# Performance work log

Hardware: AMD Instinct MI355X
Metric: run time of the kernel (lower is better)

Reference implementation:

```python
import jax, jax.numpy as jnp
import numpy as np

IFZ = 256      # in_features
SFZ = 1280     # sequence_features
AHZ = 8        # attention heads
AFZ = 64       # attention feature dim per head
NRES = 20      # canonical_num_residues
SCALE = float(np.sqrt(AFZ))
RESID = float(np.sqrt(2.0))
EPS = 1e-6


def _ln(x, s, b, eps=1e-5):
    m = jnp.mean(x, axis=-1, keepdims=True)
    v = jnp.var(x, axis=-1, keepdims=True)
    return (x - m) / jnp.sqrt(v + eps) * s + b


def setup_inputs() -> dict:
    key = jax.random.key(0)
    ks = jax.random.split(key, 20)
    N, B, S = 4096, 4, 512
    HD = AHZ * AFZ
    w = lambda k, shp: (jax.random.normal(k, shp, jnp.float32) * 0.02)
    d = {}
    d["x"] = jax.random.normal(ks[0], (N, IFZ), jnp.float32)
    d["packed_sequence_emb"] = jax.random.normal(ks[1], (B, S, SFZ), jnp.float32)
    d["packed_sequence_mask"] = jnp.ones((B, S), jnp.float32)
    d["prot_mask"] = jnp.arange(N, dtype=jnp.int32)
    d["batch"] = jax.random.randint(ks[2], (N,), 0, B, jnp.int32)
    # projections (bias=False)
    d["Wq"] = w(ks[3], (HD, IFZ))
    d["Wk"] = w(ks[4], (HD, SFZ))
    d["Wv"] = w(ks[5], (HD, SFZ))
    # ag: LayerNorm(HD) -> Linear(HD, IFZ, bias=False) (dropout = identity at eval)
    d["ag_ln_s"] = jnp.ones((HD,), jnp.float32)
    d["ag_ln_b"] = jnp.zeros((HD,), jnp.float32)
    d["Wag"] = w(ks[6], (IFZ, HD))
    d["res_ln_s"] = jnp.ones((3, IFZ), jnp.float32)
    d["res_ln_b"] = jnp.zeros((3, IFZ), jnp.float32)
    d["res_w1"] = w(ks[7], (3, IFZ, IFZ))
    d["res_b1"] = jnp.zeros((3, IFZ), jnp.float32)
    d["res_w2"] = w(ks[8], (3, IFZ, IFZ))
    d["res_b2"] = jnp.zeros((3, IFZ), jnp.float32)
    d["head_w"] = w(ks[9], (NRES, IFZ))
    d["head_b"] = jnp.zeros((NRES,), jnp.float32)
    # output LayerNorm en
    d["en_s"] = jnp.ones((IFZ,), jnp.float32)
    d["en_b"] = jnp.zeros((IFZ,), jnp.float32)
    return d


def _forward(x, emb, mask, prot_mask, batch, Wq, Wk, Wv, ag_ln_s, ag_ln_b, Wag,
             res_ln_s, res_ln_b, res_w1, res_b1, res_w2, res_b2,
             head_w, head_b, en_s, en_b):
    N = x.shape[0]
    B, S = emb.shape[:2]
    b_idx = batch[prot_mask]                      # [M]
    xp = x[prot_mask]                             # [M, IFZ]
    M = xp.shape[0]
    q = (xp @ Wq.T).reshape(M, AHZ, AFZ)          # [M,H,D]
    k = (emb @ Wk.T).reshape(B, S, AHZ, AFZ)      # [B,S,H,D]
    v = (emb @ Wv.T).reshape(B, S, AHZ, AFZ)
    # score vs every protein, then pick own protein (avoids materializing [M,S,H,D] gather)
    scores_all = jnp.einsum('mhd,bshd->mbsh', q, k) / SCALE          # [M,B,S,H]
    sel = b_idx[:, None, None, None]
    scores = jnp.take_along_axis(scores_all, sel, axis=1)[:, 0]       # [M,S,H]
    mb = mask[b_idx][:, :, None]                                      # [M,S,1]
    # padded_sequence_softmax: softmax over S, zero pads, renormalize
    sm = jax.nn.softmax(scores, axis=1) * mb
    w = sm / (jnp.sum(sm, axis=1, keepdims=True) + EPS)               # [M,S,H]
    feat_all = jnp.einsum('msh,bshd->mbhd', w, v)                     # [M,B,H,D]
    feat = jnp.take_along_axis(feat_all, sel, axis=1)[:, 0]
    feat = feat.reshape(M, AHZ * AFZ)
    ag = _ln(feat, ag_ln_s, ag_ln_b) @ Wag.T                          # [M, IFZ]
    # seq_aa_head on the scattered new features (identical to ag for unique prot_mask)
    h = ag
    for i in range(3):
        y = _ln(h, res_ln_s[i], res_ln_b[i])
        y = jax.nn.relu(y @ res_w1[i].T + res_b1[i])
        y = y @ res_w2[i].T + res_b2[i]
        h = (h + y) / RESID
    logits = h @ head_w.T + head_b                                     # [M, NRES]
    new_features = jnp.zeros_like(x).at[prot_mask].set(ag)
    seq_aa_logits = jnp.zeros((N, NRES), x.dtype).at[prot_mask].set(logits)
    unpacked_scores = jnp.zeros((N, S, AHZ), x.dtype).at[prot_mask].set(scores)
    out_x = _ln(x + new_features / RESID, en_s, en_b)
    return out_x, seq_aa_logits, unpacked_scores


def reference(x, packed_sequence_emb, packed_sequence_mask, prot_mask, batch,
              Wq, Wk, Wv, ag_ln_s, ag_ln_b, Wag,
              res_ln_s, res_ln_b, res_w1, res_b1, res_w2, res_b2,
              head_w, head_b, en_s, en_b):
    return _forward(x, packed_sequence_emb, packed_sequence_mask, prot_mask, batch,
                    Wq, Wk, Wv, ag_ln_s, ag_ln_b, Wag,
                    res_ln_s, res_ln_b, res_w1, res_b1, res_w2, res_b2,
                    head_w, head_b, en_s, en_b)
```

## Files before the change

### kernel.cpp

```cpp
#include <hip/hip_runtime.h>
#include <math.h>


typedef short bf8 __attribute__((ext_vector_type(8)));
typedef short bf4 __attribute__((ext_vector_type(4)));
typedef float f32x4 __attribute__((ext_vector_type(4)));
typedef unsigned short u16;

constexpr int LDT = 40;
enum { EPI_NONE = 0, EPI_BIAS_RELU = 1, EPI_BIAS = 2, EPI_RESID = 3 };
#define RSQRT2 0.70710678118654752f

__device__ __forceinline__ u16 f2bf(float f) {
  unsigned int u = __builtin_bit_cast(unsigned int, f);
  unsigned int r = u + 0x7fffu + ((u >> 16) & 1u);
  return (u16)(r >> 16);
}
__device__ __forceinline__ float bf2f(u16 v) {
  return __builtin_bit_cast(float, (unsigned int)v << 16);
}
__device__ __forceinline__ f32x4 mfma16(bf8 a, bf8 b, f32x4 c) {
  return __builtin_amdgcn_mfma_f32_16x16x32_bf16(a, b, c, 0, 0, 0);
}

struct CvtDesc { const float* src; u16* dst; int n; };
struct CvtArgs { CvtDesc d[8]; };

__global__ __launch_bounds__(256) void cvt_k(CvtArgs a) {
  CvtDesc d = a.d[blockIdx.z];
  int i = (blockIdx.x * 256 + threadIdx.x) * 8;
  if (i >= d.n) return;
  f32x4 v0 = *(const f32x4*)(d.src + i);
  f32x4 v1 = *(const f32x4*)(d.src + i + 4);
  bf8 o;
  o[0] = (short)f2bf(v0[0]); o[1] = (short)f2bf(v0[1]);
  o[2] = (short)f2bf(v0[2]); o[3] = (short)f2bf(v0[3]);
  o[4] = (short)f2bf(v1[0]); o[5] = (short)f2bf(v1[1]);
  o[6] = (short)f2bf(v1[2]); o[7] = (short)f2bf(v1[3]);
  *(bf8*)(d.dst + i) = o;
}

template <int EPI, bool BFOUT, int MT>
__global__ __launch_bounds__(256) void mgemm2(
    const u16* __restrict__ A, const u16* __restrict__ B,
    void* __restrict__ Cv, int M, int N, int K, int lda, int ldb, int ldc,
    const float* __restrict__ bias, const float* __restrict__ Hin,
    const int* __restrict__ gatherA, const int* __restrict__ scatterC) {
  constexpr int NF = MT / 32;
  __shared__ __align__(16) u16 As[MT * LDT];
  __shared__ __align__(16) u16 Bs[64 * LDT];
  const int tid = threadIdx.x;
  const int m0 = blockIdx.y * MT, n0 = blockIdx.x * 64;
  const int wave = tid >> 6, lane = tid & 63;
  const int wm = (wave & 1) * (MT / 2), wn = (wave >> 1) * 32;
  const int lrow = lane & 15, quad = lane >> 4;
  const int srow = tid >> 2, skq = tid & 3;

  int gr0 = m0 + srow;
  int ar0 = (gr0 < M) ? (gatherA ? gatherA[gr0] : gr0) : -1;
  const u16* Ap0 = (ar0 >= 0) ? A + (size_t)ar0 * lda + skq * 8 : nullptr;
  const u16* Ap1 = nullptr;
  if constexpr (MT == 128) {
    int gr1 = m0 + srow + 64;
    int ar1 = (gr1 < M) ? (gatherA ? gatherA[gr1] : gr1) : -1;
    Ap1 = (ar1 >= 0) ? A + (size_t)ar1 * lda + skq * 8 : nullptr;
  }
  const u16* Bp = (n0 + srow < N) ? B + (size_t)(n0 + srow) * ldb + skq * 8 : nullptr;
  u16* AsW0 = &As[srow * LDT + skq * 8];
  u16* AsW1 = (MT == 128) ? &As[(srow + 64) * LDT + skq * 8] : nullptr;
  u16* BsW = &Bs[srow * LDT + skq * 8];

  f32x4 acc[NF][2];
#pragma unroll
  for (int i = 0; i < NF; ++i)
#pragma unroll
    for (int j = 0; j < 2; ++j) acc[i][j] = (f32x4){0.f, 0.f, 0.f, 0.f};
  const bf8 z8 = {0, 0, 0, 0, 0, 0, 0, 0};

  for (int k0 = 0; k0 < K; k0 += 32) {
    bf8 a0 = Ap0 ? *(const bf8*)(Ap0 + k0) : z8;
    bf8 bv = Bp ? *(const bf8*)(Bp + k0) : z8;
    *(bf8*)AsW0 = a0;
    if constexpr (MT == 128) {
      bf8 a1 = Ap1 ? *(const bf8*)(Ap1 + k0) : z8;
      *(bf8*)AsW1 = a1;
    }
    *(bf8*)BsW = bv;
    __syncthreads();
    bf8 af[NF], bfr[2];
#pragma unroll
    for (int i = 0; i < NF; ++i)
      af[i] = *(const bf8*)&As[(wm + i * 16 + lrow) * LDT + quad * 8];
#pragma unroll
    for (int j = 0; j < 2; ++j)
      bfr[j] = *(const bf8*)&Bs[(wn + j * 16 + lrow) * LDT + quad * 8];
#pragma unroll
    for (int i = 0; i < NF; ++i)
#pragma unroll
      for (int j = 0; j < 2; ++j) acc[i][j] = mfma16(af[i], bfr[j], acc[i][j]);
    __syncthreads();
  }

  float* Cf = (float*)Cv;
  u16* Cb = (u16*)Cv;
#pragma unroll
  for (int i = 0; i < NF; ++i) {
#pragma unroll
    for (int r = 0; r < 4; ++r) {
      int row = m0 + wm + i * 16 + quad * 4 + r;
      if (row >= M) continue;
      if (gatherA && gatherA[row] < 0) continue;
      int orow = scatterC ? scatterC[row] : row;
#pragma unroll
      for (int j = 0; j < 2; ++j) {
        int col = n0 + wn + j * 16 + lrow;
        if (col >= N) continue;
        float v = acc[i][j][r];
        if (EPI == EPI_BIAS_RELU) v = fmaxf(v + bias[col], 0.f);
        else if (EPI == EPI_BIAS) v += bias[col];
        else if (EPI == EPI_RESID) v = (Hin[(size_t)row * ldc + col] + v + bias[col]) * RSQRT2;
        if (BFOUT) Cb[(size_t)orow * ldc + col] = f2bf(v);
        else Cf[(size_t)orow * ldc + col] = v;
      }
    }
  }
}

__global__ __launch_bounds__(256) void vtrans(const u16* __restrict__ KV,
                                              u16* __restrict__ VT) {
  __shared__ u16 t[32][33];
  int b = blockIdx.z;
  int s0 = blockIdx.x * 32, d0 = blockIdx.y * 32;
  int tx = threadIdx.x & 31, ty = threadIdx.x >> 5;
#pragma unroll
  for (int i = 0; i < 32; i += 8)
    t[ty + i][tx] = KV[(size_t)(b * 512 + s0 + ty + i) * 1024 + 512 + d0 + tx];
  __syncthreads();
#pragma unroll
  for (int i = 0; i < 32; i += 8)
    VT[(size_t)(b * 512 + d0 + ty + i) * 512 + s0 + tx] = t[tx][ty + i];
}

constexpr int WST = 520;
constexpr int QST = 72;

__global__ __launch_bounds__(256) void attn_fused(
    const u16* __restrict__ Q, const u16* __restrict__ KV,
    const u16* __restrict__ VT, const int* __restrict__ list,
    const float* __restrict__ mask, u16* __restrict__ packed,
    u16* __restrict__ feat, int N) {
  const int NMT = gridDim.x;
  const int lin = blockIdx.y * NMT + blockIdx.x;
  const int xcd = lin & 7, rest = lin >> 3;
  const int mt = rest % NMT;
  const int y = ((rest / NMT) << 3) | xcd;
  const int b = y >> 3, h = y & 7;
  const int* lst = list + (size_t)b * N + mt * 32;
  if (lst[0] < 0) return;

  __shared__ __align__(16) u16 Ws[32 * WST];
  __shared__ __align__(16) u16 Qs[32 * QST];
  __shared__ __align__(16) u16 KVs[64 * QST];
  __shared__ __align__(16) float mk[8][68];
  __shared__ int mS[32];

  const int tid = threadIdx.x;
  const int wave = tid >> 6, lane = tid & 63;
  const int wm = (wave & 1) * 16, wns = (wave >> 1) * 32;
  const int lrow = lane & 15, quad = lane >> 4;
  const bf8 z8 = {0, 0, 0, 0, 0, 0, 0, 0};

  const int c0 = tid * 2, c1 = tid * 2 + 1;
  const int sr0 = c0 >> 3, kq0 = c0 & 7;
  const int sr1 = c1 >> 3, kq1 = c1 & 7;
  u16* kvw0 = &KVs[sr0 * QST + kq0 * 8];
  u16* kvw1 = &KVs[sr1 * QST + kq1 * 8];

  if (tid < 32) mS[tid] = lst[tid];
  {
    int p = tid >> 5, j = (tid & 31) * 2;
    *(float2*)&mk[p][j] = *(const float2*)&mask[(size_t)b * 512 + p * 64 + j];
  }
  {
    int qr = tid >> 3, kq = tid & 7;
    int m = lst[qr];
    *(bf8*)&Qs[qr * QST + kq * 8] =
        (m >= 0) ? *(const bf8*)(Q + (size_t)m * 512 + h * 64 + kq * 8) : z8;
  }
  const u16* KVb = KV + (size_t)(b * 512) * 1024 + h * 64;
  {
    int sta = mt & 7;
    *(bf8*)kvw0 = *(const bf8*)(KVb + (size_t)(sta * 64 + sr0) * 1024 + kq0 * 8);
    *(bf8*)kvw1 = *(const bf8*)(KVb + (size_t)(sta * 64 + sr1) * 1024 + kq1 * 8);
  }
  __syncthreads();

  const bf8 qa0 = *(const bf8*)&Qs[(wm + lrow) * QST + 0 + quad * 8];
  const bf8 qa1 = *(const bf8*)&Qs[(wm + lrow) * QST + 32 + quad * 8];

  bf8 r0, r1;
  for (int st = 0; st < 8; ++st) {
    const int sta = (st + mt) & 7;
    if (st < 7) {
      int nx = (st + 1 + mt) & 7;
      r0 = *(const bf8*)(KVb + (size_t)(nx * 64 + sr0) * 1024 + kq0 * 8);
      r1 = *(const bf8*)(KVb + (size_t)(nx * 64 + sr1) * 1024 + kq1 * 8);
    }
    f32x4 acc0 = {0.f, 0.f, 0.f, 0.f}, acc1 = acc0;
    {
      bf8 b00 = *(const bf8*)&KVs[(wns + lrow) * QST + quad * 8];
      bf8 b10 = *(const bf8*)&KVs[(wns + 16 + lrow) * QST + quad * 8];
      bf8 b01 = *(const bf8*)&KVs[(wns + lrow) * QST + 32 + quad * 8];
      bf8 b11 = *(const bf8*)&KVs[(wns + 16 + lrow) * QST + 32 + quad * 8];
      __builtin_amdgcn_s_setprio(1);
      acc0 = mfma16(qa0, b00, acc0);
      acc1 = mfma16(qa0, b10, acc1);
      acc0 = mfma16(qa1, b01, acc0);
      acc1 = mfma16(qa1, b11, acc1);
      __builtin_amdgcn_s_setprio(0);
    }
#pragma unroll
    for (int r = 0; r < 4; ++r) {
      int lr = wm + quad * 4 + r;
      Ws[lr * WST + sta * 64 + wns + lrow] = f2bf(acc0[r] * 0.125f);
      Ws[lr * WST + sta * 64 + wns + 16 + lrow] = f2bf(acc1[r] * 0.125f);
    }
    __syncthreads();
    if (st < 7) {
      *(bf8*)kvw0 = r0;
      *(bf8*)kvw1 = r1;
      __syncthreads();
    }
  }

  const u16* VTb = VT + (size_t)(b * 512 + h * 64) * 512;
  bf8 v0p = *(const bf8*)(VTb + (size_t)sr0 * 512 + ((mt & 7) << 6) + kq0 * 8);
  bf8 v1p = *(const bf8*)(VTb + (size_t)sr1 * 512 + ((mt & 7) << 6) + kq1 * 8);

  {
    const int row = tid >> 3, part = tid & 7;
    u16* wrow = &Ws[row * WST + part * 64];
    const int mm = mS[row];
    bf8 w[8];
    float mx = -1e30f;
#pragma unroll
    for (int v = 0; v < 8; ++v) {
      w[v] = *(const bf8*)(wrow + v * 8);
#pragma unroll
      for (int j = 0; j < 8; ++j) mx = fmaxf(mx, bf2f((u16)w[v][j]));
    }
    if (mm >= 0) {
      u16* prow = packed + ((size_t)h * N + mm) * 512 + part * 64;
#pragma unroll
      for (int v = 0; v < 8; ++v) *(bf8*)(prow + v * 8) = w[v];
    }
#pragma unroll
    for (int d = 1; d < 8; d <<= 1) mx = fmaxf(mx, __shfl_xor(mx, d));
    float ev[64];
    float se = 0.f, ms = 0.f;
#pragma unroll
    for (int v = 0; v < 8; ++v) {
      f32x4 m0 = *(const f32x4*)&mk[part][v * 8];
      f32x4 m1 = *(const f32x4*)&mk[part][v * 8 + 4];
#pragma unroll
      for (int j = 0; j < 8; ++j) {
        float e = __expf(bf2f((u16)w[v][j]) - mx);
        ev[v * 8 + j] = e;
        se += e;
        ms += e * (j < 4 ? m0[j] : m1[j - 4]);
      }
    }
#pragma unroll
    for (int d = 1; d < 8; d <<= 1) {
      se += __shfl_xor(se, d);
      ms += __shfl_xor(ms, d);
    }
    float iv = 1.0f / (ms + 1e-6f * se);
#pragma unroll
    for (int v = 0; v < 8; ++v) {
      f32x4 m0 = *(const f32x4*)&mk[part][v * 8];
      f32x4 m1 = *(const f32x4*)&mk[part][v * 8 + 4];
      bf8 o;
#pragma unroll
      for (int j = 0; j < 8; ++j)
        o[j] = (short)f2bf(ev[v * 8 + j] * (j < 4 ? m0[j] : m1[j - 4]) * iv);
      *(bf8*)(wrow + v * 8) = o;
    }
  }
  __syncthreads();
  *(bf8*)kvw0 = v0p;
  *(bf8*)kvw1 = v1p;
  __syncthreads();

  f32x4 acc0 = {0.f, 0.f, 0.f, 0.f}, acc1 = acc0;
  for (int ss = 0; ss < 8; ++ss) {
    const int s0 = ((ss + mt) & 7) << 6;
    if (ss < 7) {
      int nx = ((ss + 1 + mt) & 7) << 6;
      v0p = *(const bf8*)(VTb + (size_t)sr0 * 512 + nx + kq0 * 8);
      v1p = *(const bf8*)(VTb + (size_t)sr1 * 512 + nx + kq1 * 8);
    }
#pragma unroll
    for (int k0 = 0; k0 < 64; k0 += 32) {
      bf8 a = *(const bf8*)&Ws[(wm + lrow) * WST + s0 + k0 + quad * 8];
      bf8 b0 = *(const bf8*)&KVs[(wns + lrow) * QST + k0 + quad * 8];
      bf8 b1 = *(const bf8*)&KVs[(wns + 16 + lrow) * QST + k0 + quad * 8];
      __builtin_amdgcn_s_setprio(1);
      acc0 = mfma16(a, b0, acc0);
      acc1 = mfma16(a, b1, acc1);
      __builtin_amdgcn_s_setprio(0);
    }
    __syncthreads();
    if (ss < 7) {
      *(bf8*)kvw0 = v0p;
      *(bf8*)kvw1 = v1p;
      __syncthreads();
    }
  }
#pragma unroll
  for (int r = 0; r < 4; ++r) {
    int lr = wm + quad * 4 + r;
    int mm = mS[lr];
    if (mm < 0) continue;
    u16* frow = feat + (size_t)mm * 512 + h * 64;
    frow[wns + lrow] = f2bf(acc0[r]);
    frow[wns + 16 + lrow] = f2bf(acc1[r]);
  }
}

constexpr int HST = 268;
constexpr int AST = 520;
constexpr int YST = 280;
constexpr int SMEM_BYTES = 16 * HST * 4 + 16 * AST * 2 + 16 * YST * 2;

__global__ __launch_bounds__(1024) void mlp_unpack(
    const u16* __restrict__ feat, const float* __restrict__ ag_s,
    const float* __restrict__ ag_b, const u16* __restrict__ Wag,
    const float* __restrict__ x, const float* __restrict__ ens,
    const float* __restrict__ enb, const float* __restrict__ rls,
    const float* __restrict__ rlb, const u16* __restrict__ rw1,
    const float* __restrict__ rb1, const u16* __restrict__ rw2,
    const float* __restrict__ rb2, const float* __restrict__ hw,
    const float* __restrict__ hb, const int* __restrict__ pm,
    const u16* __restrict__ packed, float* __restrict__ out_sc,
    float* __restrict__ out_lg, float* __restrict__ out_x,
    int nmlp, int N) {
  __shared__ __align__(16) char smem[SMEM_BYTES];
  const int tid = threadIdx.x;

  if (blockIdx.x >= nmlp) {
    u16* Ls = (u16*)smem;
    const int g = tid >> 8, t = tid & 255;
    const int m = (blockIdx.x - nmlp) * 4 + g;
    u16* Lg = Ls + g * (8 * 520);
    int h = t >> 5, c = (t & 31) * 16;
    const u16* row = packed + ((size_t)h * N + m) * 512 + c;
    *(bf8*)&Lg[h * 520 + c] = *(const bf8*)row;
    *(bf8*)&Lg[h * 520 + c + 8] = *(const bf8*)(row + 8);
    __syncthreads();
    float* orow = out_sc + (size_t)pm[m] * 4096;
#pragma unroll
    for (int i = 0; i < 16; ++i) {
      int e = t + i * 256;
      orow[e] = bf2f(Lg[(e & 7) * 520 + (e >> 3)]);
    }
    return;
  }

  float* Hs = (float*)smem;
  u16* As = (u16*)(smem + 16 * HST * 4);
  u16* Ys = (u16*)(smem + 16 * HST * 4 + 16 * AST * 2);
  const int m0 = blockIdx.x * 16;
  const int wave = tid >> 6, lane = tid & 63;
  const int lrow = lane & 15, quad = lane >> 4;
  const int wn = wave * 16;
  const int row = wave;
  const int wq8 = quad * 8;
  const int nrow = pm[m0 + row];

  const u16* WagW = Wag + (size_t)(wn + lrow) * 512 + wq8;
  const u16* W1W = rw1 + (size_t)(wn + lrow) * 256 + wq8;
  const u16* W2W = rw2 + (size_t)(wn + lrow) * 256 + wq8;

  bf8 wp[8];
#pragma unroll
  for (int i = 0; i < 8; ++i) wp[i] = *(const bf8*)(WagW + i * 32);

  {
    const u16* frow = feat + (size_t)(m0 + row) * 512 + lane * 8;
    bf8 f0 = *(const bf8*)frow;
    float s = 0.f, sq = 0.f;
#pragma unroll
    for (int j = 0; j < 8; ++j) {
      float a = bf2f((u16)f0[j]);
      s += a;
      sq += a * a;
    }
#pragma unroll
    for (int d = 1; d < 64; d <<= 1) { s += __shfl_xor(s, d); sq += __shfl_xor(sq, d); }
    float mean = s * (1.0f / 512.0f);
    float var = sq * (1.0f / 512.0f) - mean * mean;
    float is = 1.0f / sqrtf(var + 1e-5f);
    int c = lane * 8;
    bf8 o0;
#pragma unroll
    for (int j = 0; j < 8; ++j)
      o0[j] = (short)f2bf((bf2f((u16)f0[j]) - mean) * is * ag_s[c + j] + ag_b[c + j]);
    *(bf8*)&As[row * AST + c] = o0;
  }
  __syncthreads();

  {
    f32x4 acc = {0.f, 0.f, 0.f, 0.f};
#pragma unroll
    for (int i = 0; i < 8; ++i) {
      bf8 a = *(const bf8*)&As[lrow * AST + i * 32 + wq8];
      acc = mfma16(a, wp[i], acc);
      wp[i] = *(const bf8*)(WagW + 256 + i * 32);
    }
#pragma unroll
    for (int i = 0; i < 8; ++i) {
      bf8 a = *(const bf8*)&As[lrow * AST + 256 + i * 32 + wq8];
      acc = mfma16(a, wp[i], acc);
      wp[i] = *(const bf8*)(W1W + i * 32);
    }
#pragma unroll
    for (int r = 0; r < 4; ++r) {
      int rr = quad * 4 + r;
      Hs[rr * HST + wn + lrow] = acc[r];
    }
  }
  __syncthreads();

  {
    int c = lane * 4;
    f32x4 xv = *(const f32x4*)&x[(size_t)nrow * 256 + c];
    f32x4 hv = *(const f32x4*)&Hs[row * HST + c];
    f32x4 v;
#pragma unroll
    for (int e = 0; e < 4; ++e) v[e] = xv[e] + hv[e] * RSQRT2;
    float s = v[0] + v[1] + v[2] + v[3];
    float sq = v[0] * v[0] + v[1] * v[1] + v[2] * v[2] + v[3] * v[3];
#pragma unroll
    for (int d = 1; d < 64; d <<= 1) { s += __shfl_xor(s, d); sq += __shfl_xor(sq, d); }
    float mean = s * (1.0f / 256.0f);
    float var = sq * (1.0f / 256.0f) - mean * mean;
    float is = 1.0f / sqrtf(var + 1e-5f);
    f32x4 o;
#pragma unroll
    for (int e = 0; e < 4; ++e)
      o[e] = (v[e] - mean) * is * ens[c + e] + enb[c + e];
    *(f32x4*)&out_x[(size_t)nrow * 256 + c] = o;
  }

  for (int layer = 0; layer < 3; ++layer) {
    {
      int c = lane * 4;
      f32x4 h0 = *(const f32x4*)&Hs[row * HST + c];
      float s = h0[0] + h0[1] + h0[2] + h0[3];
      float sq = h0[0] * h0[0] + h0[1] * h0[1] + h0[2] * h0[2] + h0[3] * h0[3];
#pragma unroll
      for (int d = 1; d < 64; d <<= 1) { s += __shfl_xor(s, d); sq += __shfl_xor(sq, d); }
      float mean = s * (1.0f / 256.0f);
      float var = sq * (1.0f / 256.0f) - mean * mean;
      float is = 1.0f / sqrtf(var + 1e-5f);
      const float* g = rls + layer * 256;
      const float* bb = rlb + layer * 256;
      bf4 o;
#pragma unroll
      for (int e = 0; e < 4; ++e)
        o[e] = (short)f2bf((h0[e] - mean) * is * g[c + e] + bb[c + e]);
      *(bf4*)&As[row * AST + c] = o;
    }
    __syncthreads();

    {
      f32x4 acc = {0.f, 0.f, 0.f, 0.f};
#pragma unroll
      for (int i = 0; i < 8; ++i) {
        bf8 a = *(const bf8*)&As[lrow * AST + i * 32 + wq8];
        acc = mfma16(a, wp[i], acc);
        wp[i] = *(const bf8*)(W2W + (size_t)layer * 65536 + i * 32);
      }
      float bi = rb1[layer * 256 + wn + lrow];
#pragma unroll
      for (int r = 0; r < 4; ++r) {
        int rr = quad * 4 + r;
        Ys[rr * YST + wn + lrow] = f2bf(fmaxf(acc[r] + bi, 0.f));
      }
    }
    __syncthreads();

    {
      f32x4 acc = {0.f, 0.f, 0.f, 0.f};
#pragma unroll
      for (int i = 0; i < 8; ++i) {
        bf8 a = *(const bf8*)&Ys[lrow * YST + i * 32 + wq8];
        acc = mfma16(a, wp[i], acc);
        if (layer < 2)
          wp[i] = *(const bf8*)(W1W + (size_t)(layer + 1) * 65536 + i * 32);
      }
      float bi = rb2[layer * 256 + wn + lrow];
#pragma unroll
      for (int r = 0; r < 4; ++r) {
        int rr = quad * 4 + r;
        float* h0 = &Hs[rr * HST + wn + lrow];
        *h0 = (*h0 + acc[r] + bi) * RSQRT2;
      }
    }
    __syncthreads();
  }

  if (lane < 20) {
    const float* hrow = &Hs[row * HST];
    const float* wrow = hw + (size_t)lane * 256;
    float l0 = 0.f, l1 = 0.f, l2 = 0.f, l3 = 0.f;
    for (int k = 0; k < 256; k += 16) {
      f32x4 h0 = *(const f32x4*)&hrow[k];
      f32x4 h1 = *(const f32x4*)&hrow[k + 4];
      f32x4 h2 = *(const f32x4*)&hrow[k + 8];
      f32x4 h3 = *(const f32x4*)&hrow[k + 12];
      f32x4 w0 = *(const f32x4*)&wrow[k];
      f32x4 w1 = *(const f32x4*)&wrow[k + 4];
      f32x4 w2 = *(const f32x4*)&wrow[k + 8];
      f32x4 w3 = *(const f32x4*)&wrow[k + 12];
#pragma unroll
      for (int e = 0; e < 4; ++e) {
        l0 += h0[e] * w0[e];
        l1 += h1[e] * w1[e];
        l2 += h2[e] * w2[e];
        l3 += h3[e] * w3[e];
      }
    }
    out_lg[(size_t)nrow * 20 + lane] = l0 + l1 + l2 + l3 + hb[lane];
  }
}

__global__ __launch_bounds__(256) void outx_k(
    const float* __restrict__ x, const int* __restrict__ inv,
    const float* __restrict__ g, const float* __restrict__ bb,
    float* __restrict__ out) {
  __shared__ float red[256];
  int n = blockIdx.x, tid = threadIdx.x;
  if (inv[n] >= 0) return;
  float v = x[(size_t)n * 256 + tid];
  red[tid] = v;
  __syncthreads();
  for (int off = 128; off; off >>= 1) {
    if (tid < off) red[tid] += red[tid + off];
    __syncthreads();
  }
  float mean = red[0] * (1.0f / 256.0f);
  __syncthreads();
  red[tid] = v * v;
  __syncthreads();
  for (int off = 128; off; off >>= 1) {
    if (tid < off) red[tid] += red[tid + off];
    __syncthreads();
  }
  float var = red[0] * (1.0f / 256.0f) - mean * mean;
  float is = 1.0f / sqrtf(var + 1e-5f);
  out[(size_t)n * 256 + tid] = (v - mean) * is * g[tid] + bb[tid];
}

__global__ void init_idx_k(int* __restrict__ list, int* __restrict__ inv,
                           int* __restrict__ cnt, int N, int B) {
  int i = blockIdx.x * 256 + threadIdx.x;
  if (i < B * N) list[i] = -1;
  if (i < N) inv[i] = -1;
  if (i < B) cnt[i] = 0;
}

__global__ void compact_k(const int* __restrict__ pm,
                          const int* __restrict__ batch, int* __restrict__ list,
                          int* __restrict__ inv, int* __restrict__ cnt, int N) {
  int m = blockIdx.x * 256 + threadIdx.x;
  if (m >= N) return;
  int p = pm[m];
  int b = batch[p];
  int slot = atomicAdd(&cnt[b], 1);
  list[(size_t)b * N + slot] = m;
  inv[p] = m;
}

extern "C" void kernel_launch(void* const* d_in, const int* in_sizes, int n_in,
                              void* d_out, int out_size, void* d_ws,
                              size_t ws_size, hipStream_t stream) {
  const float* x = (const float*)d_in[0];
  const float* emb = (const float*)d_in[1];
  const float* mask = (const float*)d_in[2];
  const int* pm = (const int*)d_in[3];
  const int* batch = (const int*)d_in[4];
  const float* Wq = (const float*)d_in[5];
  const float* Wk = (const float*)d_in[6];
  const float* Wv = (const float*)d_in[7];
  const float* ag_s = (const float*)d_in[8];
  const float* ag_b = (const float*)d_in[9];
  const float* Wag = (const float*)d_in[10];
  const float* rls = (const float*)d_in[11];
  const float* rlb = (const float*)d_in[12];
  const float* rw1 = (const float*)d_in[13];
  const float* rb1 = (const float*)d_in[14];
  const float* rw2 = (const float*)d_in[15];
  const float* rb2 = (const float*)d_in[16];
  const float* hw = (const float*)d_in[17];
  const float* hb = (const float*)d_in[18];
  const float* ens = (const float*)d_in[19];
  const float* enb = (const float*)d_in[20];

  const int N = in_sizes[0] / 256;
  const int B = in_sizes[2] / 512;

  char* wsb = (char*)d_ws;
  u16* embbf = (u16*)(wsb + 0);
  u16* xbf   = (u16*)(wsb + 5242880);
  u16* Wkvbf = (u16*)(wsb + 7340032);
  u16* Wqbf  = (u16*)(wsb + 9961472);
  u16* packed = (u16*)(wsb + 0);
  u16* KVbf   = (u16*)(wsb + 33554432);
  u16* Qbf    = (u16*)(wsb + 37748736);
  u16* VT     = (u16*)(wsb + 41943040);
  u16* featE  = (u16*)(wsb + 44040192);
  u16* Wagbf = (u16*)(wsb + 48234496);
  u16* rw1bf = (u16*)(wsb + 48496640);
  u16* rw2bf = (u16*)(wsb + 48889856);
  int* list  = (int*)(wsb + 49545216);
  int* inv   = (int*)(wsb + 49610752);
  int* cnt   = (int*)(wsb + 49627136);

  float* out_x = (float*)d_out;
  float* out_lg = out_x + (size_t)N * 256;
  float* out_sc = out_lg + (size_t)N * 20;

  CvtArgs ca;
  ca.d[0] = {emb, embbf, 2 * 512 * 1280 * 2};
  ca.d[1] = {x, xbf, 4096 * 256};
  ca.d[2] = {Wk, Wkvbf, 512 * 1280};
  ca.d[3] = {Wv, Wkvbf + 512 * 1280, 512 * 1280};
  ca.d[4] = {Wq, Wqbf, 512 * 256};
  ca.d[5] = {Wag, Wagbf, 256 * 512};
  ca.d[6] = {rw1, rw1bf, 3 * 256 * 256};
  ca.d[7] = {rw2, rw2bf, 3 * 256 * 256};
  cvt_k<<<dim3(1281, 1, 8), 256, 0, stream>>>(ca);
  init_idx_k<<<(B * N + 255) / 256, 256, 0, stream>>>(list, inv, cnt, N, B);
  compact_k<<<(N + 255) / 256, 256, 0, stream>>>(pm, batch, list, inv, cnt, N);

  mgemm2<EPI_NONE, true, 64><<<dim3(16, B * 8), 256, 0, stream>>>(
      embbf, Wkvbf, KVbf, B * 512, 1024, 1280, 1280, 1280, 1024,
      nullptr, nullptr, nullptr, nullptr);
  mgemm2<EPI_NONE, true, 64><<<dim3(8, N / 64), 256, 0, stream>>>(
      xbf, Wqbf, Qbf, N, 512, 256, 256, 256, 512,
      nullptr, nullptr, pm, nullptr);
  vtrans<<<dim3(16, 16, B), 256, 0, stream>>>(KVbf, VT);

  attn_fused<<<dim3(N / 32, B * 8), 256, 0, stream>>>(
      Qbf, KVbf, VT, list, mask, packed, featE, N);

  const int nmlp = N / 16;
  const int nunp = N / 4;
  mlp_unpack<<<dim3(nmlp + nunp), 1024, 0, stream>>>(
      featE, ag_s, ag_b, Wagbf, x, ens, enb, rls, rlb, rw1bf, rb1,
      rw2bf, rb2, hw, hb, pm, packed, out_sc, out_lg, out_x, nmlp, N);

  outx_k<<<N, 256, 0, stream>>>(x, inv, ens, enb, out_x);
}
```

Measured before the change: 283.4 us.

## Merge conversion, compaction, and Q/KV projection launches; double-buffer projection GEMM

Folds the compaction step into the bf16 conversion kernel through a flattened block index, so there are fewer launches and no wasted 1281x8 grid. The K/V and Q projections now run as one kernel, and its GEMM body double-buffers shared memory with register prefetch of the next K slice. outx_k now uses a grid-stride loop over 64 blocks instead of launching one block per row. The compaction atomics still depend on init_idx_k having run first. Together these cut launch overhead and idle blocks, at the cost of more complex indexing and a second LDS buffer.

New measurement: 284.2 us. About the same (+0.3%).

```diff
diff --git a/kernel.cpp b/kernel.cpp
--- a/kernel.cpp
+++ b/kernel.cpp
@@ -8,7 +8,6 @@
 typedef unsigned short u16;
 
 constexpr int LDT = 40;
-enum { EPI_NONE = 0, EPI_BIAS_RELU = 1, EPI_BIAS = 2, EPI_RESID = 3 };
 #define RSQRT2 0.70710678118654752f
 
 __device__ __forceinline__ u16 f2bf(float f) {
@@ -24,105 +23,137 @@
 }
 
 struct CvtDesc { const float* src; u16* dst; int n; };
-struct CvtArgs { CvtDesc d[8]; };
-
-__global__ __launch_bounds__(256) void cvt_k(CvtArgs a) {
-  CvtDesc d = a.d[blockIdx.z];
-  int i = (blockIdx.x * 256 + threadIdx.x) * 8;
-  if (i >= d.n) return;
-  f32x4 v0 = *(const f32x4*)(d.src + i);
-  f32x4 v1 = *(const f32x4*)(d.src + i + 4);
+struct CvtArgs { CvtDesc d[8]; int blk0[9]; };
+
+__global__ __launch_bounds__(256) void cvt_k(
+    CvtArgs a, const int* __restrict__ pm, const int* __restrict__ batch,
+    int* __restrict__ list, int* __restrict__ inv, int* __restrict__ cnt,
+    int N) {
+  const int blk = blockIdx.x;
+  if (blk >= a.blk0[8]) {
+    int m = (blk - a.blk0[8]) * 256 + threadIdx.x;
+    if (m >= N) return;
+    int p = pm[m];
+    int b = batch[p];
+    int slot = atomicAdd(&cnt[b], 1);
+    list[(size_t)b * N + slot] = m;
+    inv[p] = m;
+    return;
+  }
+  int d = 0;
+#pragma unroll
+  for (int k = 1; k < 8; ++k)
+    if (blk >= a.blk0[k]) d = k;
+  CvtDesc dd = a.d[d];
+  int i = ((blk - a.blk0[d]) * 256 + threadIdx.x) * 8;
+  if (i >= dd.n) return;
+  f32x4 v0 = *(const f32x4*)(dd.src + i);
+  f32x4 v1 = *(const f32x4*)(dd.src + i + 4);
   bf8 o;
   o[0] = (short)f2bf(v0[0]); o[1] = (short)f2bf(v0[1]);
   o[2] = (short)f2bf(v0[2]); o[3] = (short)f2bf(v0[3]);
   o[4] = (short)f2bf(v1[0]); o[5] = (short)f2bf(v1[1]);
   o[6] = (short)f2bf(v1[2]); o[7] = (short)f2bf(v1[3]);
-  *(bf8*)(d.dst + i) = o;
-}
-
-template <int EPI, bool BFOUT, int MT>
-__global__ __launch_bounds__(256) void mgemm2(
+  *(bf8*)(dd.dst + i) = o;
+}
+
+__global__ void init_idx_k(int* __restrict__ list, int* __restrict__ inv,
+                           int* __restrict__ cnt, int N, int B) {
+  int i = blockIdx.x * 256 + threadIdx.x;
+  if (i < B * N) list[i] = -1;
+  if (i < N) inv[i] = -1;
+  if (i < B) cnt[i] = 0;
+}
+
+__device__ __forceinline__ void proj64_body(
+    u16 (*As)[64 * LDT], u16 (*Bs)[64 * LDT],
     const u16* __restrict__ A, const u16* __restrict__ B,
-    void* __restrict__ Cv, int M, int N, int K, int lda, int ldb, int ldc,
-    const float* __restrict__ bias, const float* __restrict__ Hin,
-    const int* __restrict__ gatherA, const int* __restrict__ scatterC) {
-  constexpr int NF = MT / 32;
-  __shared__ __align__(16) u16 As[MT * LDT];
-  __shared__ __align__(16) u16 Bs[64 * LDT];
+    u16* __restrict__ C, int M, int Nn, int K, int lda, int ldb, int ldc,
+    const int* __restrict__ gatherA, int m0, int n0) {
   const int tid = threadIdx.x;
-  const int m0 = blockIdx.y * MT, n0 = blockIdx.x * 64;
   const int wave = tid >> 6, lane = tid & 63;
-  const int wm = (wave & 1) * (MT / 2), wn = (wave >> 1) * 32;
+  const int wm = (wave & 1) * 32, wn = (wave >> 1) * 32;
   const int lrow = lane & 15, quad = lane >> 4;
   const int srow = tid >> 2, skq = tid & 3;
+  const bf8 z8 = {0, 0, 0, 0, 0, 0, 0, 0};
+  const int off = srow * LDT + skq * 8;
 
   int gr0 = m0 + srow;
   int ar0 = (gr0 < M) ? (gatherA ? gatherA[gr0] : gr0) : -1;
   const u16* Ap0 = (ar0 >= 0) ? A + (size_t)ar0 * lda + skq * 8 : nullptr;
-  const u16* Ap1 = nullptr;
-  if constexpr (MT == 128) {
-    int gr1 = m0 + srow + 64;
-    int ar1 = (gr1 < M) ? (gatherA ? gatherA[gr1] : gr1) : -1;
-    Ap1 = (ar1 >= 0) ? A + (size_t)ar1 * lda + skq * 8 : nullptr;
-  }
-  const u16* Bp = (n0 + srow < N) ? B + (size_t)(n0 + srow) * ldb + skq * 8 : nullptr;
-  u16* AsW0 = &As[srow * LDT + skq * 8];
-  u16* AsW1 = (MT == 128) ? &As[(srow + 64) * LDT + skq * 8] : nullptr;
-  u16* BsW = &Bs[srow * LDT + skq * 8];
-
-  f32x4 acc[NF][2];
-#pragma unroll
-  for (int i = 0; i < NF; ++i)
+  const u16* Bp = (n0 + srow < Nn) ? B + (size_t)(n0 + srow) * ldb + skq * 8 : nullptr;
+
+  {
+    bf8 a0 = Ap0 ? *(const bf8*)Ap0 : z8;
+    bf8 bv = Bp ? *(const bf8*)Bp : z8;
+    *(bf8*)&As[0][off] = a0;
+    *(bf8*)&Bs[0][off] = bv;
+  }
+  __syncthreads();
+
+  f32x4 acc[2][2];
+#pragma unroll
+  for (int i = 0; i < 2; ++i)
 #pragma unroll
     for (int j = 0; j < 2; ++j) acc[i][j] = (f32x4){0.f, 0.f, 0.f, 0.f};
-  const bf8 z8 = {0, 0, 0, 0, 0, 0, 0, 0};
-
+
+  int cur = 0;
   for (int k0 = 0; k0 < K; k0 += 32) {
-    bf8 a0 = Ap0 ? *(const bf8*)(Ap0 + k0) : z8;
-    bf8 bv = Bp ? *(const bf8*)(Bp + k0) : z8;
-    *(bf8*)AsW0 = a0;
-    if constexpr (MT == 128) {
-      bf8 a1 = Ap1 ? *(const bf8*)(Ap1 + k0) : z8;
-      *(bf8*)AsW1 = a1;
-    }
-    *(bf8*)BsW = bv;
-    __syncthreads();
-    bf8 af[NF], bfr[2];
-#pragma unroll
-    for (int i = 0; i < NF; ++i)
-      af[i] = *(const bf8*)&As[(wm + i * 16 + lrow) * LDT + quad * 8];
-#pragma unroll
-    for (int j = 0; j < 2; ++j)
-      bfr[j] = *(const bf8*)&Bs[(wn + j * 16 + lrow) * LDT + quad * 8];
-#pragma unroll
-    for (int i = 0; i < NF; ++i)
-#pragma unroll
-      for (int j = 0; j < 2; ++j) acc[i][j] = mfma16(af[i], bfr[j], acc[i][j]);
-    __syncthreads();
-  }
-
-  float* Cf = (float*)Cv;
-  u16* Cb = (u16*)Cv;
-#pragma unroll
-  for (int i = 0; i < NF; ++i) {
+    const bool more = (k0 + 32 < K);
+    bf8 na, nb;
+    if (more) {
+      na = Ap0 ? *(const bf8*)(Ap0 + k0 + 32) : z8;
+      nb = Bp ? *(const bf8*)(Bp + k0 + 32) : z8;
+    }
+    bf8 af0 = *(const bf8*)&As[cur][(wm + lrow) * LDT + quad * 8];
+    bf8 af1 = *(const bf8*)&As[cur][(wm + 16 + lrow) * LDT + quad * 8];
+    bf8 bf0 = *(const bf8*)&Bs[cur][(wn + lrow) * LDT + quad * 8];
+    bf8 bf1 = *(const bf8*)&Bs[cur][(wn + 16 + lrow) * LDT + quad * 8];
+    acc[0][0] = mfma16(af0, bf0, acc[0][0]);
+    acc[0][1] = mfma16(af0, bf1, acc[0][1]);
+    acc[1][0] = mfma16(af1, bf0, acc[1][0]);
+    acc[1][1] = mfma16(af1, bf1, acc[1][1]);
+    if (more) {
+      *(bf8*)&As[cur ^ 1][off] = na;
+      *(bf8*)&Bs[cur ^ 1][off] = nb;
+    }
+    __syncthreads();
+    cur ^= 1;
+  }
+
+#pragma unroll
+  for (int i = 0; i < 2; ++i)
 #pragma unroll
     for (int r = 0; r < 4; ++r) {
       int row = m0 + wm + i * 16 + quad * 4 + r;
       if (row >= M) continue;
       if (gatherA && gatherA[row] < 0) continue;
-      int orow = scatterC ? scatterC[row] : row;
 #pragma unroll
       for (int j = 0; j < 2; ++j) {
         int col = n0 + wn + j * 16 + lrow;
-        if (col >= N) continue;
-        float v = acc[i][j][r];
-        if (EPI == EPI_BIAS_RELU) v = fmaxf(v + bias[col], 0.f);
-        else if (EPI == EPI_BIAS) v += bias[col];
-        else if (EPI == EPI_RESID) v = (Hin[(size_t)row * ldc + col] + v + bias[col]) * RSQRT2;
-        if (BFOUT) Cb[(size_t)orow * ldc + col] = f2bf(v);
-        else Cf[(size_t)orow * ldc + col] = v;
+        if (col >= Nn) continue;
+        C[(size_t)row * ldc + col] = f2bf(acc[i][j][r]);
       }
     }
+}
+
+__global__ __launch_bounds__(256) void qkvproj_k(
+    const u16* __restrict__ embbf, const u16* __restrict__ Wkvbf,
+    u16* __restrict__ KVbf, const u16* __restrict__ xbf,
+    const u16* __restrict__ Wqbf, u16* __restrict__ Qbf,
+    const int* __restrict__ pm, int MKV, int N, int nkv) {
+  __shared__ __align__(16) u16 As[2][64 * LDT];
+  __shared__ __align__(16) u16 Bs[2][64 * LDT];
+  const int blk = blockIdx.x;
+  if (blk < nkv) {
+    int by = blk >> 4, bx = blk & 15;
+    proj64_body(As, Bs, embbf, Wkvbf, KVbf, MKV, 1024, 1280, 1280, 1280, 1024,
+                nullptr, by * 64, bx * 64);
+  } else {
+    int t = blk - nkv;
+    int by = t >> 3, bx = t & 7;
+    proj64_body(As, Bs, xbf, Wqbf, Qbf, N, 512, 256, 256, 256, 512,
+                pm, by * 64, bx * 64);
   }
 }
 
@@ -539,48 +570,32 @@
 __global__ __launch_bounds__(256) void outx_k(
     const float* __restrict__ x, const int* __restrict__ inv,
     const float* __restrict__ g, const float* __restrict__ bb,
-    float* __restrict__ out) {
+    float* __restrict__ out, int N) {
   __shared__ float red[256];
-  int n = blockIdx.x, tid = threadIdx.x;
-  if (inv[n] >= 0) return;
-  float v = x[(size_t)n * 256 + tid];
-  red[tid] = v;
-  __syncthreads();
-  for (int off = 128; off; off >>= 1) {
-    if (tid < off) red[tid] += red[tid + off];
-    __syncthreads();
-  }
-  float mean = red[0] * (1.0f / 256.0f);
-  __syncthreads();
-  red[tid] = v * v;
-  __syncthreads();
-  for (int off = 128; off; off >>= 1) {
-    if (tid < off) red[tid] += red[tid + off];
-    __syncthreads();
-  }
-  float var = red[0] * (1.0f / 256.0f) - mean * mean;
-  float is = 1.0f / sqrtf(var + 1e-5f);
-  out[(size_t)n * 256 + tid] = (v - mean) * is * g[tid] + bb[tid];
-}
-
-__global__ void init_idx_k(int* __restrict__ list, int* __restrict__ inv,
-                           int* __restrict__ cnt, int N, int B) {
-  int i = blockIdx.x * 256 + threadIdx.x;
-  if (i < B * N) list[i] = -1;
-  if (i < N) inv[i] = -1;
-  if (i < B) cnt[i] = 0;
-}
-
-__global__ void compact_k(const int* __restrict__ pm,
-                          const int* __restrict__ batch, int* __restrict__ list,
-                          int* __restrict__ inv, int* __restrict__ cnt, int N) {
-  int m = blockIdx.x * 256 + threadIdx.x;
-  if (m >= N) return;
-  int p = pm[m];
-  int b = batch[p];
-  int slot = atomicAdd(&cnt[b], 1);
-  list[(size_t)b * N + slot] = m;
-  inv[p] = m;
+  int tid = threadIdx.x;
+  for (int n = blockIdx.x; n < N; n += gridDim.x) {
+    if (inv[n] >= 0) continue;
+    __syncthreads();
+    float v = x[(size_t)n * 256 + tid];
+    red[tid] = v;
+    __syncthreads();
+    for (int off = 128; off; off >>= 1) {
+      if (tid < off) red[tid] += red[tid + off];
+      __syncthreads();
+    }
+    float mean = red[0] * (1.0f / 256.0f);
+    __syncthreads();
+    red[tid] = v * v;
+    __syncthreads();
+    for (int off = 128; off; off >>= 1) {
+      if (tid < off) red[tid] += red[tid + off];
+      __syncthreads();
+    }
+    float var = red[0] * (1.0f / 256.0f) - mean * mean;
+    float is = 1.0f / sqrtf(var + 1e-5f);
+    out[(size_t)n * 256 + tid] = (v - mean) * is * g[tid] + bb[tid];
+    __syncthreads();
+  }
 }
 
 extern "C" void kernel_launch(void* const* d_in, const int* in_sizes, int n_in,
@@ -632,8 +647,9 @@
   float* out_lg = out_x + (size_t)N * 256;
   float* out_sc = out_lg + (size_t)N * 20;
 
+  init_idx_k<<<(B * N + 255) / 256, 256, 0, stream>>>(list, inv, cnt, N, B);
   CvtArgs ca;
-  ca.d[0] = {emb, embbf, 2 * 512 * 1280 * 2};
+  ca.d[0] = {emb, embbf, B * 512 * 1280};
   ca.d[1] = {x, xbf, 4096 * 256};
   ca.d[2] = {Wk, Wkvbf, 512 * 1280};
   ca.d[3] = {Wv, Wkvbf + 512 * 1280, 512 * 1280};
@@ -641,16 +657,21 @@
   ca.d[5] = {Wag, Wagbf, 256 * 512};
   ca.d[6] = {rw1, rw1bf, 3 * 256 * 256};
   ca.d[7] = {rw2, rw2bf, 3 * 256 * 256};
-  cvt_k<<<dim3(1281, 1, 8), 256, 0, stream>>>(ca);
-  init_idx_k<<<(B * N + 255) / 256, 256, 0, stream>>>(list, inv, cnt, N, B);
-  compact_k<<<(N + 255) / 256, 256, 0, stream>>>(pm, batch, list, inv, cnt, N);
-
-  mgemm2<EPI_NONE, true, 64><<<dim3(16, B * 8), 256, 0, stream>>>(
-      embbf, Wkvbf, KVbf, B * 512, 1024, 1280, 1280, 1280, 1024,
-      nullptr, nullptr, nullptr, nullptr);
-  mgemm2<EPI_NONE, true, 64><<<dim3(8, N / 64), 256, 0, stream>>>(
-      xbf, Wqbf, Qbf, N, 512, 256, 256, 256, 512,
-      nullptr, nullptr, pm, nullptr);
+  {
+    int acc = 0;
+    for (int k = 0; k < 8; ++k) {
+      ca.blk0[k] = acc;
+      acc += (ca.d[k].n / 8 + 255) / 256;
+    }
+    ca.blk0[8] = acc;
+    const int ncompact = (N + 255) / 256;
+    cvt_k<<<acc + ncompact, 256, 0, stream>>>(ca, pm, batch, list, inv, cnt, N);
+  }
+
+  const int nkv = (B * 512 / 64) * 16;
+  const int nq = (N / 64) * 8;
+  qkvproj_k<<<nkv + nq, 256, 0, stream>>>(
+      embbf, Wkvbf, KVbf, xbf, Wqbf, Qbf, pm, B * 512, N, nkv);
   vtrans<<<dim3(16, 16, B), 256, 0, stream>>>(KVbf, VT);
 
   attn_fused<<<dim3(N / 32, B * 8), 256, 0, stream>>>(
@@ -662,5 +683,5 @@
       featE, ag_s, ag_b, Wagbf, x, ens, enb, rls, rlb, rw1bf, rb1,
       rw2bf, rb2, hw, hb, pm, packed, out_sc, out_lg, out_x, nmlp, N);
 
-  outx_k<<<N, 256, 0, stream>>>(x, inv, ens, enb, out_x);
-}
+  outx_k<<<64, 256, 0, stream>>>(x, inv, ens, enb, out_x, N);
+}
```
